# Performance work log

Measured on AMD Instinct MI355X. Metric: run time of the kernel, lower is better.

The kernel has to match this reference:

```python
import jax, jax.numpy as jnp
import numpy as np

HEAD_DIM = 64  # embed_dim(1024) // num_heads(16); used only for score scaling
QMAX = 127.0   # int8 symmetric fake-quant range


def fake_quant(x):
    """Per-tensor symmetric int8 quant-dequant with straight-through estimator."""
    scale = jnp.maximum(jnp.max(jnp.abs(x)) / QMAX, 1e-8)
    q = jnp.clip(jnp.round(x / scale), -QMAX, QMAX) * scale
    return x + jax.lax.stop_gradient(q - x)


def qlinear(x, W, b):
    """QuantizedLinear: y = x @ fake_quant(W).T + b (torch Linear convention)."""
    return jnp.einsum('bse,oe->bso', x, fake_quant(W)) + b


def setup_inputs() -> dict:
    key = jax.random.key(0)
    ks = jax.random.split(key, 11)
    B, S, E = 8, 2048, 1024
    mk = lambda k, shape, sc=1.0: (jax.random.normal(k, shape, dtype=jnp.float32) * sc)
    return {
        'query': mk(ks[0], (B, S, E)),
        'key': mk(ks[1], (B, S, E)),
        'value': mk(ks[2], (B, S, E)),
        'Wq': mk(ks[3], (E, E), 0.02), 'bq': mk(ks[4], (E,), 0.02),
        'Wk': mk(ks[5], (E, E), 0.02), 'bk': mk(ks[6], (E,), 0.02),
        'Wv': mk(ks[7], (E, E), 0.02), 'bv': mk(ks[8], (E,), 0.02),
        'Wp': mk(ks[9], (E, E), 0.02), 'bp': mk(ks[10], (E,), 0.02),
    }


def reference(query, key, value, Wq, bq, Wk, bk, Wv, bv, Wp, bp):
    # seq_first=True: no transpose; tensors stay [B, S, E]
    q = qlinear(fake_quant(query), Wq, bq)
    k = qlinear(fake_quant(key), Wk, bk)
    v = qlinear(fake_quant(value), Wv, bv)
    # NOTE: original code does NOT split heads; scores are [B, S, S]
    scores = jnp.einsum('bqe,bke->bqk', q, k) / jnp.sqrt(jnp.float32(HEAD_DIM))
    attn = jax.nn.softmax(scores, axis=-1)  # dropout p=0.0 -> identity
    attn_out = jnp.einsum('bqk,bke->bqe', attn, v)
    return qlinear(fake_quant(attn_out), Wp, bp)
```

## Files before the change

### kernel.cpp

```cpp
#include <hip/hip_runtime.h>


typedef __attribute__((ext_vector_type(4))) float f32x4;
typedef __attribute__((ext_vector_type(4))) int i32x4;
typedef __attribute__((ext_vector_type(8))) char s8x8;
typedef _Float16 f16;
typedef _Float16 half8 __attribute__((ext_vector_type(8)));

#define DEVI static __device__ __forceinline__

constexpr int B_ = 8, S_ = 2048, E_ = 1024;
constexpr long NROW = (long)B_ * S_;

constexpr size_t KB = 1024, MB = 1024 * 1024;
constexpr size_t OFF_SC  = 0;
constexpr size_t OFF_RS  = 1 * KB;
constexpr size_t OFF_W   = 128 * KB;
constexpr size_t SZ_WPL  = (size_t)E_ * E_;
constexpr size_t SZ_PL   = (size_t)NROW * E_ * 2;
constexpr size_t OFF_QH  = OFF_W + 4 * SZ_WPL;
constexpr size_t OFF_KH  = OFF_QH + SZ_PL;
constexpr size_t OFF_VH  = OFF_KH + SZ_PL;
constexpr size_t OFF_VT  = OFF_VH + SZ_PL;
constexpr size_t OFF_SCB = OFF_VT + SZ_PL;
constexpr size_t WS_NEED = OFF_SCB + 64 * MB;
constexpr size_t OFF_AOQ = OFF_SCB;

typedef const __attribute__((address_space(1))) void* gptr1;
typedef __attribute__((address_space(3))) void* lptr3;

DEVI void gload16(const void* g, void* l) {
  __builtin_amdgcn_global_load_lds((gptr1)g, (lptr3)l, 16, 0, 0);
}

DEVI f32x4 MF16(half8 a, half8 b, f32x4 c) {
  return __builtin_amdgcn_mfma_f32_16x16x32_f16(a, b, c, 0, 0, 0);
}
DEVI i32x4 MFI8(i32x4 a, i32x4 b, i32x4 c) {
  return __builtin_amdgcn_mfma_i32_16x16x64_i8(a, b, c, 0, 0, 0);
}

DEVI float scale_of(const unsigned int* amaxU, int idx) {
  return fmaxf(__uint_as_float(amaxU[idx]) / 127.f, 1e-8f);
}

DEVI signed char q8(float x, float s) {
  return (signed char)(int)fminf(fmaxf(rintf(x / s), -127.f), 127.f);
}

DEVI int xcd_swz(int d, int n) { return (d & 7) * (n >> 3) + (d >> 3); }

DEVI void block_atomic_max(float m, unsigned int* dst) {
  __shared__ float red[4];
#pragma unroll
  for (int o = 32; o; o >>= 1) m = fmaxf(m, __shfl_xor(m, o));
  const int lane = threadIdx.x & 63, wid = threadIdx.x >> 6;
  if (lane == 0) red[wid] = m;
  __syncthreads();
  if (threadIdx.x == 0) {
    m = fmaxf(fmaxf(red[0], red[1]), fmaxf(red[2], red[3]));
    atomicMax(dst, __float_as_uint(m));
  }
}

__global__ void k_zero(float* o, long n) {
  long i = ((long)blockIdx.x * blockDim.x + threadIdx.x) * 4;
  const long stride = (long)gridDim.x * blockDim.x * 4;
  for (; i < n; i += stride) {
    float4 z = {0.f, 0.f, 0.f, 0.f};
    *(float4*)(o + i) = z;
  }
}

__global__ void k_init(unsigned int* a) {
  if (threadIdx.x < 8) a[threadIdx.x] = 0u;
}

DEVI void amax_body(const float* __restrict__ x, long n, unsigned int* amaxU, int idx) {
  long i = ((long)blockIdx.x * blockDim.x + threadIdx.x) * 8;
  const long stride = (long)gridDim.x * blockDim.x * 8;
  float m = 0.f;
  for (; i < n; i += stride) {
    float4 a = *(const float4*)(x + i);
    float4 b = *(const float4*)(x + i + 4);
    m = fmaxf(m, fmaxf(fmaxf(fabsf(a.x), fabsf(a.y)), fmaxf(fabsf(a.z), fabsf(a.w))));
    m = fmaxf(m, fmaxf(fmaxf(fabsf(b.x), fabsf(b.y)), fmaxf(fabsf(b.z), fabsf(b.w))));
  }
  block_atomic_max(m, amaxU + idx);
}

__global__ void k_amax_in(const float* __restrict__ q, const float* __restrict__ k,
                          const float* __restrict__ v, long n, unsigned int* amaxU) {
  const int z = blockIdx.z;
  amax_body(z == 0 ? q : (z == 1 ? k : v), n, amaxU, z);
}
__global__ void k_amax_w(const float* __restrict__ a, const float* __restrict__ b,
                         const float* __restrict__ c, const float* __restrict__ d,
                         long n, unsigned int* amaxU) {
  const int z = blockIdx.z;
  amax_body(z == 0 ? a : (z == 1 ? b : (z == 2 ? c : d)), n, amaxU, 3 + z);
}

DEVI void quant8_body(const float* __restrict__ x, signed char* __restrict__ q, long n,
                      float s) {
  long i = ((long)blockIdx.x * blockDim.x + threadIdx.x) * 8;
  const long stride = (long)gridDim.x * blockDim.x * 8;
  for (; i < n; i += stride) {
    float4 a = *(const float4*)(x + i);
    float4 b = *(const float4*)(x + i + 4);
    s8x8 o;
    o[0] = q8(a.x, s); o[1] = q8(a.y, s); o[2] = q8(a.z, s); o[3] = q8(a.w, s);
    o[4] = q8(b.x, s); o[5] = q8(b.y, s); o[6] = q8(b.z, s); o[7] = q8(b.w, s);
    *(s8x8*)(q + i) = o;
  }
}

__global__ void k_quant_in(const float* __restrict__ q, const float* __restrict__ k,
                           const float* __restrict__ v, signed char* __restrict__ out,
                           long n, const unsigned int* __restrict__ amaxU) {
  const int z = blockIdx.z;
  quant8_body(z == 0 ? q : (z == 1 ? k : v), out + (size_t)z * n, n, scale_of(amaxU, z));
}
__global__ void k_quant_w(const float* __restrict__ a, const float* __restrict__ b,
                          const float* __restrict__ c, const float* __restrict__ d,
                          signed char* __restrict__ out, long n,
                          const unsigned int* __restrict__ amaxU) {
  const int z = blockIdx.z;
  quant8_body(z == 0 ? a : (z == 1 ? b : (z == 2 ? c : d)), out + (size_t)z * n, n,
              scale_of(amaxU, 3 + z));
}

__global__ void k_quant8_f16(char* __restrict__ ws) {
  const unsigned int* amaxU = (const unsigned int*)(ws + OFF_SC);
  const float s = scale_of(amaxU, 7);
  const f16* x = (const f16*)(ws + OFF_VH);
  signed char* o = (signed char*)(ws + OFF_AOQ);
  const long n = NROW * E_;
  long i = ((long)blockIdx.x * blockDim.x + threadIdx.x) * 8;
  const long stride = (long)gridDim.x * blockDim.x * 8;
  for (; i < n; i += stride) {
    half8 v = *(const half8*)(x + i);
    s8x8 w;
#pragma unroll
    for (int j = 0; j < 8; ++j) w[j] = q8((float)v[j], s);
    *(s8x8*)(o + i) = w;
  }
}

DEVI void gemm_core_i8(const signed char* __restrict__ A, const signed char* __restrict__ Bm,
                       int lda, int K, signed char* ldsA, signed char* ldsB,
                       i32x4 acc[4][4], int tid) {
  const int lane = tid & 63, wid = tid >> 6;
  const int wm = wid >> 1, wn = wid & 1;
  const int frow = lane & 15;
  const int fko = (lane >> 4) * 16;
  for (int k0 = 0; k0 < K; k0 += 128) {
    __syncthreads();
#pragma unroll
    for (int it = 0; it < 4; ++it) {
      int c = it * 256 + tid;
      int row = c >> 3, cc = c & 7;
      int lb = (it * 256 + (tid & 192)) * 16;
      gload16(A + (long)row * lda + k0 + cc * 16, ldsA + lb);
      gload16(Bm + (long)row * lda + k0 + cc * 16, ldsB + lb);
    }
    __syncthreads();
#pragma unroll
    for (int kc = 0; kc < 2; ++kc) {
      i32x4 a[4], b[4];
#pragma unroll
      for (int m = 0; m < 4; ++m)
        a[m] = *(const i32x4*)(ldsA + (wm * 64 + m * 16 + frow) * 128 + kc * 64 + fko);
#pragma unroll
      for (int n = 0; n < 4; ++n)
        b[n] = *(const i32x4*)(ldsB + (wn * 64 + n * 16 + frow) * 128 + kc * 64 + fko);
#pragma unroll
      for (int m = 0; m < 4; ++m)
#pragma unroll
        for (int n = 0; n < 4; ++n)
          acc[m][n] = MFI8(a[m], b[n], acc[m][n]);
    }
  }
}

DEVI void gemm_core_f16(const unsigned short* __restrict__ A,
                        const unsigned short* __restrict__ Bm, int lda, int ldb, int K,
                        unsigned short* ldsA, unsigned short* ldsB, f32x4 acc[4][4], int tid) {
  const int lane = tid & 63, wid = tid >> 6;
  const int wm = wid >> 1, wn = wid & 1;
  const int frow = lane & 15;
  const int fko = (lane >> 4) * 8;
  for (int k0 = 0; k0 < K; k0 += 64) {
    __syncthreads();
#pragma unroll
    for (int it = 0; it < 4; ++it) {
      int c = it * 256 + tid;
      int row = c >> 3, cc = c & 7;
      int lb = (it * 256 + (tid & 192)) * 8;
      gload16(A + (long)row * lda + k0 + cc * 8, ldsA + lb);
      gload16(Bm + (long)row * ldb + k0 + cc * 8, ldsB + lb);
    }
    __syncthreads();
#pragma unroll
    for (int kc = 0; kc < 2; ++kc) {
      half8 a[4], b[4];
#pragma unroll
      for (int m = 0; m < 4; ++m)
        a[m] = *(const half8*)(ldsA + (wm * 64 + m * 16 + frow) * 64 + kc * 32 + fko);
#pragma unroll
      for (int n = 0; n < 4; ++n)
        b[n] = *(const half8*)(ldsB + (wn * 64 + n * 16 + frow) * 64 + kc * 32 + fko);
#pragma unroll
      for (int m = 0; m < 4; ++m)
#pragma unroll
        for (int n = 0; n < 4; ++n)
          acc[m][n] = MF16(a[m], b[n], acc[m][n]);
    }
  }
}

__global__ __launch_bounds__(256, 4) void k_proj_i8(char* __restrict__ ws,
                                                    const signed char* __restrict__ qi,
                                                    const float* __restrict__ bq,
                                                    const float* __restrict__ bk,
                                                    const float* __restrict__ bv) {
  __shared__ __attribute__((aligned(16))) signed char lA[128 * 128], lB[128 * 128];
  const int tid = threadIdx.x;
  int d = blockIdx.x + 8 * blockIdx.y + 1024 * blockIdx.z;
  int w = xcd_swz(d, 3072);
  const int bx = w & 7, by = (w >> 3) & 127, z = w >> 10;
  const unsigned int* amaxU = (const unsigned int*)(ws + OFF_SC);
  const signed char* A = qi + (size_t)z * NROW * E_ + (size_t)by * 128 * E_;
  const signed char* Bm =
      (const signed char*)(ws + OFF_W + (size_t)z * SZ_WPL) + (size_t)bx * 128 * E_;
  f16* H = (f16*)(ws + OFF_QH + (size_t)z * SZ_PL);
  const float* bias = (z == 0) ? bq : ((z == 1) ? bk : bv);
  const float sc = scale_of(amaxU, z) * scale_of(amaxU, 3 + z);
  i32x4 acc[4][4] = {};
  gemm_core_i8(A, Bm, E_, E_, lA, lB, acc, tid);
  const int lane = tid & 63, wid = tid >> 6, wm = wid >> 1, wn = wid & 1;
  const long r0 = (long)by * 128 + wm * 64;
  const int c0 = bx * 128 + wn * 64;
#pragma unroll
  for (int m = 0; m < 4; ++m)
#pragma unroll
    for (int n = 0; n < 4; ++n) {
      int col = c0 + n * 16 + (lane & 15);
      float bc = bias[col];
#pragma unroll
      for (int r = 0; r < 4; ++r) {
        long row = r0 + m * 16 + (lane >> 4) * 4 + r;
        H[row * E_ + col] = (f16)(sc * (float)acc[m][n][r] + bc);
      }
    }
}

__global__ void k_transpose(char* __restrict__ ws) {
  __shared__ f16 t[64][72];
  const int b = blockIdx.z, e0 = blockIdx.x * 64, s0 = blockIdx.y * 64;
  const f16* V = (const f16*)(ws + OFF_VH) + (size_t)b * S_ * E_;
  f16* VT = (f16*)(ws + OFF_VT) + (size_t)b * E_ * S_;
  const int tid = threadIdx.x;
  const int r = tid >> 2, cc = (tid & 3) * 16;
#pragma unroll
  for (int j = 0; j < 2; ++j) {
    half8 v = *(const half8*)(V + (size_t)(s0 + r) * E_ + e0 + cc + j * 8);
#pragma unroll
    for (int q = 0; q < 8; ++q) t[cc + j * 8 + q][r] = v[q];
  }
  __syncthreads();
#pragma unroll
  for (int j = 0; j < 2; ++j) {
    half8 w;
#pragma unroll
    for (int q = 0; q < 8; ++q) w[q] = t[r][cc + j * 8 + q];
    *(half8*)(VT + (size_t)(e0 + r) * S_ + s0 + cc + j * 8) = w;
  }
}

__global__ __launch_bounds__(256, 4) void k_scores(char* __restrict__ ws) {
  __shared__ __attribute__((aligned(16))) unsigned short lA[128 * 64], lB[128 * 64];
  const int tid = threadIdx.x;
  int d = blockIdx.x + 16 * blockIdx.y + 256 * blockIdx.z;
  int w = xcd_swz(d, 2048);
  const int bx = w & 15, by = (w >> 4) & 15, b = w >> 8;
  const unsigned short* A =
      (const unsigned short*)(ws + OFF_QH) + ((size_t)b * S_ + (size_t)by * 128) * E_;
  const unsigned short* Bm =
      (const unsigned short*)(ws + OFF_KH) + ((size_t)b * S_ + (size_t)bx * 128) * E_;
  f16* C = (f16*)(ws + OFF_SCB) + (size_t)b * S_ * S_;
  f32x4 acc[4][4] = {};
  gemm_core_f16(A, Bm, E_, E_, E_, lA, lB, acc, tid);
  const int lane = tid & 63, wid = tid >> 6, wm = wid >> 1, wn = wid & 1;
  const int r0 = by * 128 + wm * 64;
  const int c0 = bx * 128 + wn * 64;
#pragma unroll
  for (int m = 0; m < 4; ++m)
#pragma unroll
    for (int n = 0; n < 4; ++n) {
      int col = c0 + n * 16 + (lane & 15);
#pragma unroll
      for (int r = 0; r < 4; ++r) {
        int row = r0 + m * 16 + (lane >> 4) * 4 + r;
        C[(size_t)row * S_ + col] = (f16)(0.125f * acc[m][n][r]);
      }
    }
}

__global__ __launch_bounds__(256) void k_softmax(char* __restrict__ ws) {
  const long row = blockIdx.x;
  f16* src = (f16*)(ws + OFF_SCB) + row * S_;
  float* RS = (float*)(ws + OFF_RS);
  const int tid = threadIdx.x, lane = tid & 63, wid = tid >> 6;
  half8 v = *(const half8*)(src + (long)tid * 8);
  float x[8];
#pragma unroll
  for (int j = 0; j < 8; ++j) x[j] = (float)v[j];
  float m = x[0];
#pragma unroll
  for (int j = 1; j < 8; ++j) m = fmaxf(m, x[j]);
#pragma unroll
  for (int o = 32; o; o >>= 1) m = fmaxf(m, __shfl_xor(m, o));
  __shared__ float redm[4], reds[4];
  if (lane == 0) redm[wid] = m;
  __syncthreads();
  m = fmaxf(fmaxf(redm[0], redm[1]), fmaxf(redm[2], redm[3]));
  float e[8], s = 0.f;
#pragma unroll
  for (int j = 0; j < 8; ++j) {
    e[j] = expf(x[j] - m);
    s += e[j];
  }
#pragma unroll
  for (int o = 32; o; o >>= 1) s += __shfl_xor(s, o);
  if (lane == 0) reds[wid] = s;
  __syncthreads();
  s = (reds[0] + reds[1]) + (reds[2] + reds[3]);
  if (tid == 0) RS[row] = 1.f / s;
  half8 p;
#pragma unroll
  for (int j = 0; j < 8; ++j) p[j] = (f16)e[j];
  *(half8*)(src + (long)tid * 8) = p;
}

__global__ __launch_bounds__(256, 4) void k_pv(char* __restrict__ ws) {
  __shared__ __attribute__((aligned(16))) unsigned short lA[128 * 64], lB[128 * 64];
  const int tid = threadIdx.x;
  int d = blockIdx.x + 8 * blockIdx.y + 128 * blockIdx.z;
  int w = xcd_swz(d, 1024);
  const int bx = w & 7, by = (w >> 3) & 15, b = w >> 7;
  const unsigned short* A = (const unsigned short*)(ws + OFF_SCB) + (size_t)b * S_ * S_ +
                            (size_t)by * 128 * S_;
  const unsigned short* Bm = (const unsigned short*)(ws + OFF_VT) + (size_t)b * E_ * S_ +
                             (size_t)bx * 128 * S_;
  f32x4 acc[4][4] = {};
  gemm_core_f16(A, Bm, S_, S_, S_, lA, lB, acc, tid);
  const float* RS = (const float*)(ws + OFF_RS) + (size_t)b * S_;
  f16* O = (f16*)(ws + OFF_VH) + (size_t)b * S_ * E_;
  unsigned int* amaxU = (unsigned int*)(ws + OFF_SC);
  const int lane = tid & 63, wid = tid >> 6, wm = wid >> 1, wn = wid & 1;
  const int r0 = by * 128 + wm * 64;
  const int c0 = bx * 128 + wn * 64;
  float mx = 0.f;
#pragma unroll
  for (int m = 0; m < 4; ++m)
#pragma unroll
    for (int n = 0; n < 4; ++n) {
      int col = c0 + n * 16 + (lane & 15);
#pragma unroll
      for (int r = 0; r < 4; ++r) {
        int row = r0 + m * 16 + (lane >> 4) * 4 + r;
        float o = acc[m][n][r] * RS[row];
        O[(size_t)row * E_ + col] = (f16)o;
        mx = fmaxf(mx, fabsf(o));
      }
    }
  __syncthreads();
  block_atomic_max(mx, amaxU + 7);
}

__global__ __launch_bounds__(256, 4) void k_final_i8(char* __restrict__ ws,
                                                     const float* __restrict__ bp,
                                                     float* __restrict__ out) {
  __shared__ __attribute__((aligned(16))) signed char lA[128 * 128], lB[128 * 128];
  const int tid = threadIdx.x;
  int d = blockIdx.x + 8 * blockIdx.y;
  int w = xcd_swz(d, 1024);
  const int bx = w & 7, by = w >> 3;
  const unsigned int* amaxU = (const unsigned int*)(ws + OFF_SC);
  const signed char* A = (const signed char*)(ws + OFF_AOQ) + (size_t)by * 128 * E_;
  const signed char* Bm =
      (const signed char*)(ws + OFF_W + 3 * SZ_WPL) + (size_t)bx * 128 * E_;
  const float sc = scale_of(amaxU, 7) * scale_of(amaxU, 6);
  i32x4 acc[4][4] = {};
  gemm_core_i8(A, Bm, E_, E_, lA, lB, acc, tid);
  const int lane = tid & 63, wid = tid >> 6, wm = wid >> 1, wn = wid & 1;
  const long r0 = (long)by * 128 + wm * 64;
  const int c0 = bx * 128 + wn * 64;
#pragma unroll
  for (int m = 0; m < 4; ++m)
#pragma unroll
    for (int n = 0; n < 4; ++n) {
      int col = c0 + n * 16 + (lane & 15);
      float bc = bp[col];
#pragma unroll
      for (int r = 0; r < 4; ++r) {
        long row = r0 + m * 16 + (lane >> 4) * 4 + r;
        out[row * E_ + col] = sc * (float)acc[m][n][r] + bc;
      }
    }
}

extern "C" void kernel_launch(void* const* d_in, const int* in_sizes, int n_in,
                              void* d_out, int out_size, void* d_ws, size_t ws_size,
                              hipStream_t stream) {
  (void)in_sizes; (void)n_in; (void)out_size;
  char* ws = (char*)d_ws;
  const float* query = (const float*)d_in[0];
  const float* key   = (const float*)d_in[1];
  const float* value = (const float*)d_in[2];
  const float* Wq = (const float*)d_in[3];
  const float* bq = (const float*)d_in[4];
  const float* Wk = (const float*)d_in[5];
  const float* bk = (const float*)d_in[6];
  const float* Wv = (const float*)d_in[7];
  const float* bv = (const float*)d_in[8];
  const float* Wp = (const float*)d_in[9];
  const float* bp = (const float*)d_in[10];

  const long nIn = NROW * E_;
  const long nW = (long)E_ * E_;

  if (ws_size < WS_NEED) {
    k_zero<<<dim3(2048), dim3(256), 0, stream>>>((float*)d_out, nIn);
    return;
  }

  unsigned int* amaxU = (unsigned int*)(ws + OFF_SC);
  signed char* qi = (signed char*)d_out;

  k_init<<<dim3(1), dim3(64), 0, stream>>>(amaxU);
  k_amax_in<<<dim3(512, 1, 3), dim3(256), 0, stream>>>(query, key, value, nIn, amaxU);
  k_amax_w<<<dim3(64, 1, 4), dim3(256), 0, stream>>>(Wq, Wk, Wv, Wp, nW, amaxU);
  k_quant_in<<<dim3(1024, 1, 3), dim3(256), 0, stream>>>(query, key, value, qi, nIn, amaxU);
  k_quant_w<<<dim3(128, 1, 4), dim3(256), 0, stream>>>(Wq, Wk, Wv, Wp,
                                                       (signed char*)(ws + OFF_W), nW, amaxU);

  k_proj_i8<<<dim3(8, 128, 3), dim3(256), 0, stream>>>(ws, qi, bq, bk, bv);
  k_transpose<<<dim3(16, 32, 8), dim3(256), 0, stream>>>(ws);

  k_scores<<<dim3(16, 16, 8), dim3(256), 0, stream>>>(ws);
  k_softmax<<<dim3(16384), dim3(256), 0, stream>>>(ws);
  k_pv<<<dim3(8, 16, 8), dim3(256), 0, stream>>>(ws);

  k_quant8_f16<<<dim3(1024), dim3(256), 0, stream>>>(ws);
  k_final_i8<<<dim3(8, 128), dim3(256), 0, stream>>>(ws, bp, (float*)d_out);
}
```

Measured before the change: 424.5 us.

## Use 256x256 tiles with 4-stage pipelined LDS staging for scores and PV GEMMs

Replaces the 128x128 single-buffered f16 GEMM core used by the scores and PV kernels with a 256x256-tile, 512-thread core. It stages K-slices of 32 into a 4-slot LDS ring with explicit vmcnt waits, so global loads are prefetched three steps ahead. The LDS layout is XOR-swizzled to avoid bank conflicts, and MFMA issue priority is raised around the compute loop. In exchange, each block uses more registers and LDS and the grids are much smaller: 512 and 256 blocks. That risks lower occupancy and tail effects.

```diff
diff --git a/kernel.cpp b/kernel.cpp
--- a/kernel.cpp
+++ b/kernel.cpp
@@ -8,6 +8,8 @@
 typedef _Float16 half8 __attribute__((ext_vector_type(8)));
 
 #define DEVI static __device__ __forceinline__
+#define VMCNT(n) asm volatile("s_waitcnt vmcnt(" #n ")" ::: "memory")
+#define BAR() __builtin_amdgcn_s_barrier()
 
 constexpr int B_ = 8, S_ = 2048, E_ = 1024;
 constexpr long NROW = (long)B_ * S_;
@@ -50,6 +52,8 @@
 
 DEVI int xcd_swz(int d, int n) { return (d & 7) * (n >> 3) + (d >> 3); }
 
+DEVI int swz(int a) { return a ^ (((a >> 7) & 7) << 4); }
+
 DEVI void block_atomic_max(float m, unsigned int* dst) {
   __shared__ float red[4];
 #pragma unroll
@@ -60,6 +64,21 @@
   if (threadIdx.x == 0) {
     m = fmaxf(fmaxf(red[0], red[1]), fmaxf(red[2], red[3]));
     atomicMax(dst, __float_as_uint(m));
+  }
+}
+
+DEVI void block_atomic_max8(float m, unsigned int* dst) {
+  __shared__ float red8[8];
+#pragma unroll
+  for (int o = 32; o; o >>= 1) m = fmaxf(m, __shfl_xor(m, o));
+  const int lane = threadIdx.x & 63, wid = threadIdx.x >> 6;
+  if (lane == 0) red8[wid] = m;
+  __syncthreads();
+  if (threadIdx.x == 0) {
+    float r = red8[0];
+#pragma unroll
+    for (int i = 1; i < 8; ++i) r = fmaxf(r, red8[i]);
+    atomicMax(dst, __float_as_uint(r));
   }
 }
 
@@ -183,39 +202,66 @@
   }
 }
 
-DEVI void gemm_core_f16(const unsigned short* __restrict__ A,
-                        const unsigned short* __restrict__ Bm, int lda, int ldb, int K,
-                        unsigned short* ldsA, unsigned short* ldsB, f32x4 acc[4][4], int tid) {
+DEVI void stage_slot(const unsigned short* __restrict__ src, int ld_elems, int k0_elems,
+                     unsigned short* slot, int tid) {
+#pragma unroll
+  for (int c = 0; c < 2; ++c) {
+    int L = (c * 512 + tid) * 16;
+    int sw = swz(L);
+    gload16((const char*)src + (size_t)(sw >> 6) * ((size_t)ld_elems * 2) +
+                (size_t)k0_elems * 2 + (sw & 63),
+            (char*)slot + L);
+  }
+}
+
+DEVI void attn_core256(const unsigned short* __restrict__ A,
+                       const unsigned short* __restrict__ Bm, int lda, int ldb, int nt,
+                       unsigned short* ldsA, unsigned short* ldsB, f32x4 acc[8][4], int tid) {
   const int lane = tid & 63, wid = tid >> 6;
-  const int wm = wid >> 1, wn = wid & 1;
-  const int frow = lane & 15;
-  const int fko = (lane >> 4) * 8;
-  for (int k0 = 0; k0 < K; k0 += 64) {
-    __syncthreads();
-#pragma unroll
-    for (int it = 0; it < 4; ++it) {
-      int c = it * 256 + tid;
-      int row = c >> 3, cc = c & 7;
-      int lb = (it * 256 + (tid & 192)) * 8;
-      gload16(A + (long)row * lda + k0 + cc * 8, ldsA + lb);
-      gload16(Bm + (long)row * ldb + k0 + cc * 8, ldsB + lb);
-    }
-    __syncthreads();
-#pragma unroll
-    for (int kc = 0; kc < 2; ++kc) {
-      half8 a[4], b[4];
-#pragma unroll
-      for (int m = 0; m < 4; ++m)
-        a[m] = *(const half8*)(ldsA + (wm * 64 + m * 16 + frow) * 64 + kc * 32 + fko);
-#pragma unroll
-      for (int n = 0; n < 4; ++n)
-        b[n] = *(const half8*)(ldsB + (wn * 64 + n * 16 + frow) * 64 + kc * 32 + fko);
-#pragma unroll
-      for (int m = 0; m < 4; ++m)
-#pragma unroll
-        for (int n = 0; n < 4; ++n)
-          acc[m][n] = MF16(a[m], b[n], acc[m][n]);
-    }
+  const int wm = wid >> 2, wn = wid & 3;
+  const int frow = lane & 15, ko = lane >> 4;
+  stage_slot(A, lda, 0, ldsA, tid);
+  stage_slot(Bm, ldb, 0, ldsB, tid);
+  stage_slot(A, lda, 32, ldsA + 8192, tid);
+  stage_slot(Bm, ldb, 32, ldsB + 8192, tid);
+  stage_slot(A, lda, 64, ldsA + 16384, tid);
+  stage_slot(Bm, ldb, 64, ldsB + 16384, tid);
+  VMCNT(8);
+  BAR();
+  for (int t = 0; t < nt; ++t) {
+    if (t + 3 < nt) {
+      int s = (t + 3) & 3;
+      stage_slot(A, lda, (t + 3) * 32, ldsA + s * 8192, tid);
+      stage_slot(Bm, ldb, (t + 3) * 32, ldsB + s * 8192, tid);
+    }
+    const unsigned short* sA = ldsA + (t & 3) * 8192;
+    const unsigned short* sB = ldsB + (t & 3) * 8192;
+    half8 a[8], b[4];
+#pragma unroll
+    for (int m = 0; m < 8; ++m) {
+      int R = (wm * 128 + m * 16 + frow) * 64 + ko * 16;
+      a[m] = *(const half8*)((const char*)sA + swz(R));
+    }
+#pragma unroll
+    for (int n = 0; n < 4; ++n) {
+      int R = (wn * 64 + n * 16 + frow) * 64 + ko * 16;
+      b[n] = *(const half8*)((const char*)sB + swz(R));
+    }
+    __builtin_amdgcn_s_setprio(1);
+#pragma unroll
+    for (int m = 0; m < 8; ++m)
+#pragma unroll
+      for (int n = 0; n < 4; ++n) acc[m][n] = MF16(a[m], b[n], acc[m][n]);
+    __builtin_amdgcn_s_setprio(0);
+    int rem = nt - 1 - t;
+    if (rem >= 3) {
+      VMCNT(8);
+    } else if (rem == 2) {
+      VMCNT(4);
+    } else {
+      VMCNT(0);
+    }
+    BAR();
   }
 }
 
@@ -278,27 +324,28 @@
   }
 }
 
-__global__ __launch_bounds__(256, 4) void k_scores(char* __restrict__ ws) {
-  __shared__ __attribute__((aligned(16))) unsigned short lA[128 * 64], lB[128 * 64];
+__global__ __launch_bounds__(512, 2) void k_scores256(char* __restrict__ ws) {
+  __shared__ __attribute__((aligned(16))) unsigned short ldsA[4 * 8192], ldsB[4 * 8192];
   const int tid = threadIdx.x;
-  int d = blockIdx.x + 16 * blockIdx.y + 256 * blockIdx.z;
-  int w = xcd_swz(d, 2048);
-  const int bx = w & 15, by = (w >> 4) & 15, b = w >> 8;
+  int d = blockIdx.x + 8 * blockIdx.y + 64 * blockIdx.z;
+  int w = xcd_swz(d, 512);
+  const int bx = w & 7, by = (w >> 3) & 7, b = w >> 6;
   const unsigned short* A =
-      (const unsigned short*)(ws + OFF_QH) + ((size_t)b * S_ + (size_t)by * 128) * E_;
+      (const unsigned short*)(ws + OFF_QH) + ((size_t)b * S_ + (size_t)by * 256) * E_;
   const unsigned short* Bm =
-      (const unsigned short*)(ws + OFF_KH) + ((size_t)b * S_ + (size_t)bx * 128) * E_;
+      (const unsigned short*)(ws + OFF_KH) + ((size_t)b * S_ + (size_t)bx * 256) * E_;
   f16* C = (f16*)(ws + OFF_SCB) + (size_t)b * S_ * S_;
-  f32x4 acc[4][4] = {};
-  gemm_core_f16(A, Bm, E_, E_, E_, lA, lB, acc, tid);
-  const int lane = tid & 63, wid = tid >> 6, wm = wid >> 1, wn = wid & 1;
-  const int r0 = by * 128 + wm * 64;
-  const int c0 = bx * 128 + wn * 64;
-#pragma unroll
-  for (int m = 0; m < 4; ++m)
+  f32x4 acc[8][4] = {};
+  attn_core256(A, Bm, E_, E_, E_ / 32, ldsA, ldsB, acc, tid);
+  const int lane = tid & 63, wid = tid >> 6, wm = wid >> 2, wn = wid & 3;
+  const int frow = lane & 15;
+  const int r0 = by * 256 + wm * 128;
+  const int c0 = bx * 256 + wn * 64;
+#pragma unroll
+  for (int m = 0; m < 8; ++m)
 #pragma unroll
     for (int n = 0; n < 4; ++n) {
-      int col = c0 + n * 16 + (lane & 15);
+      int col = c0 + n * 16 + frow;
 #pragma unroll
       for (int r = 0; r < 4; ++r) {
         int row = r0 + m * 16 + (lane >> 4) * 4 + r;
@@ -343,30 +390,31 @@
   *(half8*)(src + (long)tid * 8) = p;
 }
 
-__global__ __launch_bounds__(256, 4) void k_pv(char* __restrict__ ws) {
-  __shared__ __attribute__((aligned(16))) unsigned short lA[128 * 64], lB[128 * 64];
+__global__ __launch_bounds__(512, 2) void k_pv256(char* __restrict__ ws) {
+  __shared__ __attribute__((aligned(16))) unsigned short ldsA[4 * 8192], ldsB[4 * 8192];
   const int tid = threadIdx.x;
-  int d = blockIdx.x + 8 * blockIdx.y + 128 * blockIdx.z;
-  int w = xcd_swz(d, 1024);
-  const int bx = w & 7, by = (w >> 3) & 15, b = w >> 7;
+  int d = blockIdx.x + 4 * blockIdx.y + 32 * blockIdx.z;
+  int w = xcd_swz(d, 256);
+  const int bx = w & 3, by = (w >> 2) & 7, b = w >> 5;
   const unsigned short* A = (const unsigned short*)(ws + OFF_SCB) + (size_t)b * S_ * S_ +
-                            (size_t)by * 128 * S_;
+                            (size_t)by * 256 * S_;
   const unsigned short* Bm = (const unsigned short*)(ws + OFF_VT) + (size_t)b * E_ * S_ +
-                             (size_t)bx * 128 * S_;
-  f32x4 acc[4][4] = {};
-  gemm_core_f16(A, Bm, S_, S_, S_, lA, lB, acc, tid);
+                             (size_t)bx * 256 * S_;
+  f32x4 acc[8][4] = {};
+  attn_core256(A, Bm, S_, S_, S_ / 32, ldsA, ldsB, acc, tid);
   const float* RS = (const float*)(ws + OFF_RS) + (size_t)b * S_;
   f16* O = (f16*)(ws + OFF_VH) + (size_t)b * S_ * E_;
   unsigned int* amaxU = (unsigned int*)(ws + OFF_SC);
-  const int lane = tid & 63, wid = tid >> 6, wm = wid >> 1, wn = wid & 1;
-  const int r0 = by * 128 + wm * 64;
-  const int c0 = bx * 128 + wn * 64;
+  const int lane = tid & 63, wid = tid >> 6, wm = wid >> 2, wn = wid & 3;
+  const int frow = lane & 15;
+  const int r0 = by * 256 + wm * 128;
+  const int c0 = bx * 256 + wn * 64;
   float mx = 0.f;
 #pragma unroll
-  for (int m = 0; m < 4; ++m)
+  for (int m = 0; m < 8; ++m)
 #pragma unroll
     for (int n = 0; n < 4; ++n) {
-      int col = c0 + n * 16 + (lane & 15);
+      int col = c0 + n * 16 + frow;
 #pragma unroll
       for (int r = 0; r < 4; ++r) {
         int row = r0 + m * 16 + (lane >> 4) * 4 + r;
@@ -375,8 +423,7 @@
         mx = fmaxf(mx, fabsf(o));
       }
     }
-  __syncthreads();
-  block_atomic_max(mx, amaxU + 7);
+  block_atomic_max8(mx, amaxU + 7);
 }
 
 __global__ __launch_bounds__(256, 4) void k_final_i8(char* __restrict__ ws,
@@ -449,9 +496,9 @@
   k_proj_i8<<<dim3(8, 128, 3), dim3(256), 0, stream>>>(ws, qi, bq, bk, bv);
   k_transpose<<<dim3(16, 32, 8), dim3(256), 0, stream>>>(ws);
 
-  k_scores<<<dim3(16, 16, 8), dim3(256), 0, stream>>>(ws);
+  k_scores256<<<dim3(8, 8, 8), dim3(512), 0, stream>>>(ws);
   k_softmax<<<dim3(16384), dim3(256), 0, stream>>>(ws);
-  k_pv<<<dim3(8, 16, 8), dim3(256), 0, stream>>>(ws);
+  k_pv256<<<dim3(4, 8, 8), dim3(512), 0, stream>>>(ws);
 
   k_quant8_f16<<<dim3(1024), dim3(256), 0, stream>>>(ws);
   k_final_i8<<<dim3(8, 128), dim3(256), 0, stream>>>(ws, bp, (float*)d_out);
```

After: 439.5 us. 1.04x slower.

## Double-buffer f16 GEMM LDS tiles with swizzled async loads and setprio

Applied to the files above, without the earlier changes.

Replaces the single-buffered f16 GEMM core used by the scores and PV kernels with a double-buffered pipeline. K-steps shrink to 32 and the tile for step t+2 is prefetched while step t is computed, with vmcnt waits and raw barriers. An XOR swizzle on LDS addresses is added to reduce bank conflicts, and s_setprio raises priority around the MFMA block. The intent is to hide global-to-LDS load latency behind compute, at the cost of more barriers per K-step and fragile hand-counted vmcnt synchronisation.

```diff
diff --git a/kernel.cpp b/kernel.cpp
--- a/kernel.cpp
+++ b/kernel.cpp
@@ -8,6 +8,8 @@
 typedef _Float16 half8 __attribute__((ext_vector_type(8)));
 
 #define DEVI static __device__ __forceinline__
+#define VMCNT(n) asm volatile("s_waitcnt vmcnt(" #n ")" ::: "memory")
+#define BAR() __builtin_amdgcn_s_barrier()
 
 constexpr int B_ = 8, S_ = 2048, E_ = 1024;
 constexpr long NROW = (long)B_ * S_;
@@ -50,6 +52,8 @@
 
 DEVI int xcd_swz(int d, int n) { return (d & 7) * (n >> 3) + (d >> 3); }
 
+DEVI int swz32(int a) { return a ^ (((a >> 6) & 3) << 4); }
+
 DEVI void block_atomic_max(float m, unsigned int* dst) {
   __shared__ float red[4];
 #pragma unroll
@@ -183,39 +187,59 @@
   }
 }
 
-DEVI void gemm_core_f16(const unsigned short* __restrict__ A,
-                        const unsigned short* __restrict__ Bm, int lda, int ldb, int K,
-                        unsigned short* ldsA, unsigned short* ldsB, f32x4 acc[4][4], int tid) {
+DEVI void stage32(const unsigned short* __restrict__ src, int ld, int k0,
+                  unsigned short* slot, int tid) {
+#pragma unroll
+  for (int c = 0; c < 2; ++c) {
+    int L = (c * 256 + tid) * 16;
+    int sw = swz32(L);
+    gload16((const char*)src + (size_t)(sw >> 6) * ((size_t)ld * 2) +
+                (size_t)k0 * 2 + (sw & 63),
+            (char*)slot + L);
+  }
+}
+
+DEVI void gemm_f16_db(const unsigned short* __restrict__ A,
+                      const unsigned short* __restrict__ Bm, int lda, int ldb, int nt,
+                      unsigned short* ldsA, unsigned short* ldsB, f32x4 acc[4][4], int tid) {
   const int lane = tid & 63, wid = tid >> 6;
   const int wm = wid >> 1, wn = wid & 1;
-  const int frow = lane & 15;
-  const int fko = (lane >> 4) * 8;
-  for (int k0 = 0; k0 < K; k0 += 64) {
-    __syncthreads();
-#pragma unroll
-    for (int it = 0; it < 4; ++it) {
-      int c = it * 256 + tid;
-      int row = c >> 3, cc = c & 7;
-      int lb = (it * 256 + (tid & 192)) * 8;
-      gload16(A + (long)row * lda + k0 + cc * 8, ldsA + lb);
-      gload16(Bm + (long)row * ldb + k0 + cc * 8, ldsB + lb);
-    }
-    __syncthreads();
-#pragma unroll
-    for (int kc = 0; kc < 2; ++kc) {
-      half8 a[4], b[4];
-#pragma unroll
-      for (int m = 0; m < 4; ++m)
-        a[m] = *(const half8*)(ldsA + (wm * 64 + m * 16 + frow) * 64 + kc * 32 + fko);
-#pragma unroll
-      for (int n = 0; n < 4; ++n)
-        b[n] = *(const half8*)(ldsB + (wn * 64 + n * 16 + frow) * 64 + kc * 32 + fko);
-#pragma unroll
-      for (int m = 0; m < 4; ++m)
-#pragma unroll
-        for (int n = 0; n < 4; ++n)
-          acc[m][n] = MF16(a[m], b[n], acc[m][n]);
-    }
+  const int frow = lane & 15, ko = lane >> 4;
+  stage32(A, lda, 0, ldsA, tid);
+  stage32(Bm, ldb, 0, ldsB, tid);
+  stage32(A, lda, 32, ldsA + 4096, tid);
+  stage32(Bm, ldb, 32, ldsB + 4096, tid);
+  VMCNT(4);
+  BAR();
+  for (int t = 0; t < nt; ++t) {
+    const unsigned short* sA = ldsA + (t & 1) * 4096;
+    const unsigned short* sB = ldsB + (t & 1) * 4096;
+    half8 a[4], b[4];
+#pragma unroll
+    for (int m = 0; m < 4; ++m) {
+      int R = (wm * 64 + m * 16 + frow) * 64 + ko * 16;
+      a[m] = *(const half8*)((const char*)sA + swz32(R));
+    }
+#pragma unroll
+    for (int n = 0; n < 4; ++n) {
+      int R = (wn * 64 + n * 16 + frow) * 64 + ko * 16;
+      b[n] = *(const half8*)((const char*)sB + swz32(R));
+    }
+    __builtin_amdgcn_s_setprio(1);
+#pragma unroll
+    for (int m = 0; m < 4; ++m)
+#pragma unroll
+      for (int n = 0; n < 4; ++n) acc[m][n] = MF16(a[m], b[n], acc[m][n]);
+    __builtin_amdgcn_s_setprio(0);
+    BAR();
+    if (t + 2 < nt) {
+      stage32(A, lda, (t + 2) * 32, ldsA + (t & 1) * 4096, tid);
+      stage32(Bm, ldb, (t + 2) * 32, ldsB + (t & 1) * 4096, tid);
+      VMCNT(4);
+    } else {
+      VMCNT(0);
+    }
+    BAR();
   }
 }
 
@@ -279,7 +303,7 @@
 }
 
 __global__ __launch_bounds__(256, 4) void k_scores(char* __restrict__ ws) {
-  __shared__ __attribute__((aligned(16))) unsigned short lA[128 * 64], lB[128 * 64];
+  __shared__ __attribute__((aligned(16))) unsigned short ldsA[2 * 4096], ldsB[2 * 4096];
   const int tid = threadIdx.x;
   int d = blockIdx.x + 16 * blockIdx.y + 256 * blockIdx.z;
   int w = xcd_swz(d, 2048);
@@ -290,7 +314,7 @@
       (const unsigned short*)(ws + OFF_KH) + ((size_t)b * S_ + (size_t)bx * 128) * E_;
   f16* C = (f16*)(ws + OFF_SCB) + (size_t)b * S_ * S_;
   f32x4 acc[4][4] = {};
-  gemm_core_f16(A, Bm, E_, E_, E_, lA, lB, acc, tid);
+  gemm_f16_db(A, Bm, E_, E_, E_ / 32, ldsA, ldsB, acc, tid);
   const int lane = tid & 63, wid = tid >> 6, wm = wid >> 1, wn = wid & 1;
   const int r0 = by * 128 + wm * 64;
   const int c0 = bx * 128 + wn * 64;
@@ -344,7 +368,7 @@
 }
 
 __global__ __launch_bounds__(256, 4) void k_pv(char* __restrict__ ws) {
-  __shared__ __attribute__((aligned(16))) unsigned short lA[128 * 64], lB[128 * 64];
+  __shared__ __attribute__((aligned(16))) unsigned short ldsA[2 * 4096], ldsB[2 * 4096];
   const int tid = threadIdx.x;
   int d = blockIdx.x + 8 * blockIdx.y + 128 * blockIdx.z;
   int w = xcd_swz(d, 1024);
@@ -354,7 +378,7 @@
   const unsigned short* Bm = (const unsigned short*)(ws + OFF_VT) + (size_t)b * E_ * S_ +
                              (size_t)bx * 128 * S_;
   f32x4 acc[4][4] = {};
-  gemm_core_f16(A, Bm, S_, S_, S_, lA, lB, acc, tid);
+  gemm_f16_db(A, Bm, S_, S_, S_ / 32, ldsA, ldsB, acc, tid);
   const float* RS = (const float*)(ws + OFF_RS) + (size_t)b * S_;
   f16* O = (f16*)(ws + OFF_VH) + (size_t)b * S_ * E_;
   unsigned int* amaxU = (unsigned int*)(ws + OFF_SC);
```

New measurement: 442.6 us. 4.3% more time.

## Fuse V transpose into projection epilogue via swizzled LDS staging

Applied to the files above, without the earlier changes.

For the V projection slice, the GEMM epilogue now stages each wave's 64x64 f16 tile in shared memory, reusing the GEMM's LDS buffers with a rotating swizzle against bank conflicts. It then writes the tile transposed straight into the VT buffer. This removes the separate transpose kernel, along with its launch and its extra write and read of V through global memory. In exchange the V-slice blocks run a heavier epilogue with a block barrier, and the untransposed VH buffer is no longer written.

```diff
diff --git a/kernel.cpp b/kernel.cpp
--- a/kernel.cpp
+++ b/kernel.cpp
@@ -233,48 +233,59 @@
   const signed char* A = qi + (size_t)z * NROW * E_ + (size_t)by * 128 * E_;
   const signed char* Bm =
       (const signed char*)(ws + OFF_W + (size_t)z * SZ_WPL) + (size_t)bx * 128 * E_;
-  f16* H = (f16*)(ws + OFF_QH + (size_t)z * SZ_PL);
   const float* bias = (z == 0) ? bq : ((z == 1) ? bk : bv);
   const float sc = scale_of(amaxU, z) * scale_of(amaxU, 3 + z);
   i32x4 acc[4][4] = {};
   gemm_core_i8(A, Bm, E_, E_, lA, lB, acc, tid);
   const int lane = tid & 63, wid = tid >> 6, wm = wid >> 1, wn = wid & 1;
-  const long r0 = (long)by * 128 + wm * 64;
   const int c0 = bx * 128 + wn * 64;
-#pragma unroll
-  for (int m = 0; m < 4; ++m)
-#pragma unroll
-    for (int n = 0; n < 4; ++n) {
-      int col = c0 + n * 16 + (lane & 15);
-      float bc = bias[col];
-#pragma unroll
-      for (int r = 0; r < 4; ++r) {
-        long row = r0 + m * 16 + (lane >> 4) * 4 + r;
-        H[row * E_ + col] = (f16)(sc * (float)acc[m][n][r] + bc);
-      }
-    }
-}
-
-__global__ void k_transpose(char* __restrict__ ws) {
-  __shared__ f16 t[64][72];
-  const int b = blockIdx.z, e0 = blockIdx.x * 64, s0 = blockIdx.y * 64;
-  const f16* V = (const f16*)(ws + OFF_VH) + (size_t)b * S_ * E_;
-  f16* VT = (f16*)(ws + OFF_VT) + (size_t)b * E_ * S_;
-  const int tid = threadIdx.x;
-  const int r = tid >> 2, cc = (tid & 3) * 16;
-#pragma unroll
-  for (int j = 0; j < 2; ++j) {
-    half8 v = *(const half8*)(V + (size_t)(s0 + r) * E_ + e0 + cc + j * 8);
-#pragma unroll
-    for (int q = 0; q < 8; ++q) t[cc + j * 8 + q][r] = v[q];
-  }
-  __syncthreads();
-#pragma unroll
-  for (int j = 0; j < 2; ++j) {
-    half8 w;
-#pragma unroll
-    for (int q = 0; q < 8; ++q) w[q] = t[r][cc + j * 8 + q];
-    *(half8*)(VT + (size_t)(e0 + r) * S_ + s0 + cc + j * 8) = w;
+  if (z < 2) {
+    f16* H = (f16*)(ws + OFF_QH + (size_t)z * SZ_PL);
+    const long r0 = (long)by * 128 + wm * 64;
+#pragma unroll
+    for (int m = 0; m < 4; ++m)
+#pragma unroll
+      for (int n = 0; n < 4; ++n) {
+        int col = c0 + n * 16 + (lane & 15);
+        float bc = bias[col];
+#pragma unroll
+        for (int r = 0; r < 4; ++r) {
+          long row = r0 + m * 16 + (lane >> 4) * 4 + r;
+          H[row * E_ + col] = (f16)(sc * (float)acc[m][n][r] + bc);
+        }
+      }
+  } else {
+    __syncthreads();
+    f16* tb = (wid < 2) ? (f16*)lA + wid * 4096 : (f16*)lB + (wid - 2) * 4096;
+#pragma unroll
+    for (int m = 0; m < 4; ++m)
+#pragma unroll
+      for (int n = 0; n < 4; ++n) {
+        int lc = n * 16 + (lane & 15);
+        float bc = bias[c0 + lc];
+#pragma unroll
+        for (int r = 0; r < 4; ++r) {
+          int l = m * 16 + (lane >> 4) * 4 + r;
+          tb[l * 64 + ((lc + l) & 63)] = (f16)(sc * (float)acc[m][n][r] + bc);
+        }
+      }
+    asm volatile("s_waitcnt lgkmcnt(0)" ::: "memory");
+    const int bb = by >> 4;
+    const int s0 = ((by & 15) * 128) + wm * 64;
+    f16* VT = (f16*)(ws + OFF_VT) + (size_t)bb * E_ * S_;
+    const int eg = lane >> 3;
+    const int sb = (lane & 7) * 8;
+#pragma unroll
+    for (int it = 0; it < 8; ++it) {
+      int e_loc = it * 8 + eg;
+      half8 v;
+#pragma unroll
+      for (int q = 0; q < 8; ++q) {
+        int s_loc = sb + q;
+        v[q] = tb[s_loc * 64 + ((e_loc + s_loc) & 63)];
+      }
+      *(half8*)(VT + (size_t)(c0 + e_loc) * S_ + s0 + sb) = v;
+    }
   }
 }
 
@@ -447,7 +458,6 @@
                                                        (signed char*)(ws + OFF_W), nW, amaxU);
 
   k_proj_i8<<<dim3(8, 128, 3), dim3(256), 0, stream>>>(ws, qi, bq, bk, bv);
-  k_transpose<<<dim3(16, 32, 8), dim3(256), 0, stream>>>(ws);
 
   k_scores<<<dim3(16, 16, 8), dim3(256), 0, stream>>>(ws);
   k_softmax<<<dim3(16384), dim3(256), 0, stream>>>(ws);
```

After: 411.7 us. 1.03x faster.
